# Optimization experiments

Measured on AMD Instinct MI355X. Metric: run time of the kernel, lower is better.

The kernel has to match this reference:

```python
import jax, jax.numpy as jnp
import numpy as np
from itertools import product

N = 300000          # active voxels
CIN, C = 16, 32     # input / conv channels
K = 27              # 3x3x3 kernel volume
Z, Y, X = 41, 1024, 1024  # sparse spatial shape (grid_size[::-1] + [1,0,0])
B = 2               # batch size
EPS = 1e-3          # BatchNorm eps (matches norm_fn eps=0.001)


def _build_coords_and_rulebook(rng):
    # unique active coords per batch element
    total = Z * Y * X
    per = N // B
    coords = []
    for b in range(B):
        lin = np.unique(rng.integers(0, total, size=int(per * 1.3)))
        rng.shuffle(lin)
        lin = lin[:per]
        assert lin.shape[0] == per
        z = lin // (Y * X)
        y = (lin % (Y * X)) // X
        x = lin % X
        coords.append(np.stack([np.full(per, b), z, y, x], axis=1))
    coords = np.concatenate(coords, axis=0).astype(np.int64)  # [N,4]

    # hash-free rulebook via sorted linear keys + searchsorted
    key = ((coords[:, 0] * Z + coords[:, 1]) * Y + coords[:, 2]) * X + coords[:, 3]
    perm = np.argsort(key)
    skey = key[perm]
    nbr = np.full((N, K), -1, dtype=np.int32)
    bz, zz, yy, xx = coords[:, 0], coords[:, 1], coords[:, 2], coords[:, 3]
    for k, (dz, dy, dx) in enumerate(product((-1, 0, 1), repeat=3)):
        nz, ny, nx = zz + dz, yy + dy, xx + dx
        valid = (nz >= 0) & (nz < Z) & (ny >= 0) & (ny < Y) & (nx >= 0) & (nx < X)
        nkey = ((bz * Z + nz) * Y + ny) * X + nx
        pos = np.searchsorted(skey, nkey)
        pos = np.clip(pos, 0, N - 1)
        found = valid & (skey[pos] == nkey)
        nbr[:, k] = np.where(found, perm[pos], -1).astype(np.int32)
    return coords, nbr


def _bn_params(k, c):
    k1, k2, k3, k4 = jax.random.split(k, 4)
    gamma = jax.random.uniform(k1, (c,), minval=0.5, maxval=1.5)
    beta = jax.random.normal(k2, (c,)) * 0.1
    mean = jax.random.normal(k3, (c,)) * 0.1
    var = jax.random.uniform(k4, (c,), minval=0.5, maxval=1.5)
    return jnp.stack([gamma, beta, mean, var], axis=0)  # [4,C]


def setup_inputs() -> dict:
    rng = np.random.default_rng(0)
    _, nbr = _build_coords_and_rulebook(rng)

    key = jax.random.key(0)
    ks = jax.random.split(key, 12)
    feat = jax.random.normal(ks[0], (N, CIN), dtype=jnp.float32)

    def conv_w(k, cin, cout):
        return jax.random.normal(k, (K, cin, cout), dtype=jnp.float32) * (1.0 / np.sqrt(K * cin))

    return {
        "voxel_features": feat,
        "neighbor_idx": jnp.asarray(nbr),
        "w_in": conv_w(ks[1], CIN, C), "bn_in": _bn_params(ks[2], C),
        "w1a": conv_w(ks[3], C, C), "bn1a": _bn_params(ks[4], C),
        "w1b": conv_w(ks[5], C, C), "bn1b": _bn_params(ks[6], C),
        "w2a": conv_w(ks[7], C, C), "bn2a": _bn_params(ks[8], C),
        "w2b": conv_w(ks[9], C, C), "bn2b": _bn_params(ks[10], C),
    }


def reference(voxel_features, neighbor_idx, w_in, bn_in, w1a, bn1a, w1b, bn1b,
              w2a, bn2a, w2b, bn2b):
    def bn(x, p):
        gamma, beta, mean, var = p
        return gamma * (x - mean) * jax.lax.rsqrt(var + EPS) + beta

    def subm(feat, w):
        # submanifold conv: gather active neighbors, GEMM per kernel offset, accumulate
        out = jnp.zeros((feat.shape[0], w.shape[2]), feat.dtype)
        for k in range(K):
            idx = neighbor_idx[:, k]
            g = jnp.where((idx >= 0)[:, None], feat[jnp.maximum(idx, 0)], 0.0)
            out = out + g @ w[k]
        return out

    # conv_input: SubMConv3d + BN + ReLU
    x = jax.nn.relu(bn(subm(voxel_features, w_in), bn_in))
    # conv1: two SparseBasicBlocks (conv-bn-relu-conv-bn + residual, relu)
    for wa, bna, wb, bnb in ((w1a, bn1a, w1b, bn1b), (w2a, bn2a, w2b, bn2b)):
        identity = x
        x = jax.nn.relu(bn(subm(x, wa), bna))
        x = bn(subm(x, wb), bnb)
        x = jax.nn.relu(x + identity)
    # voxel importance (vis_importance branch, minus file IO / sorting side effects)
    voxel_importance = jax.nn.sigmoid(jnp.mean(jnp.abs(x), axis=1, keepdims=True))
    return x, voxel_importance
```

## Files before the change

### kernel.cpp

```cpp
#include <hip/hip_runtime.h>
#include <hip/hip_bf16.h>
#include <hip/hip_fp16.h>
#include <cstdint>
#include <cstddef>

#define NVOX 300000
#define KNBR 27
#define COUT 32
#define CINP 32
#define NT   (NVOX / 16)
#define RB   ((NVOX + 255) / 256)
#define WFIXE (5 * KNBR * CINP * COUT)
#define WFB  ((WFIXE + 255) / 256)
#define WDE  (5 * COUT * CINP)
#define WDB  ((WDE + 255) / 256)
#define WDK  (5 * KNBR * CINP * COUT)
#define WKB  ((WDK + 255) / 256)
#define WPL  (KNBR * CINP * COUT)
#define GD   1792
#define GF0  256
#define GC1  512
#define GP   256
#define PCAP 150016

typedef __hip_bfloat16 bf16;
typedef _Float16 half8 __attribute__((ext_vector_type(8)));
typedef float floatx4 __attribute__((ext_vector_type(4)));
typedef unsigned short ushort8 __attribute__((ext_vector_type(8)));

__device__ __forceinline__ float bf2f(unsigned short u) {
    union { unsigned int i; float f; } x; x.i = ((unsigned int)u) << 16; return x.f;
}
__device__ __forceinline__ int detect_fp32(const void* b0) {
    const unsigned short* p = (const unsigned short*)b0;
    int hits = 0;
    for (int i = 0; i < 16; i++) {
        float v = bf2f(p[2 * i]);
        if (v >= 0.25f && v <= 4.0f) hits++;
    }
    return (hits >= 8) ? 0 : 1;
}
__device__ __forceinline__ float rdw(const void* w, int rel, int fp32) {
    return fp32 ? ((const float*)w)[rel] : __bfloat162float(((const bf16*)w)[rel]);
}


__global__ __launch_bounds__(256)
void setup_kernel(const int* __restrict__ nbr,
                  const void* w0, const void* w1, const void* w2, const void* w3, const void* w4,
                  const void* b0, const void* b1, const void* b2, const void* b3, const void* b4,
                  float* __restrict__ wfix, __half* __restrict__ wtf, __half* __restrict__ wtk,
                  float* __restrict__ bnab,
                  int* __restrict__ flag, int* __restrict__ counter,
                  int* __restrict__ cvlist, int* __restrict__ corrpos,
                  unsigned char* __restrict__ nnarr, int* __restrict__ pk1) {
    const int tid = threadIdx.x;

    if (blockIdx.x < RB) {
        __shared__ int flags[256];
        __shared__ int pk1s[256];
        __shared__ int wsum[4];
        __shared__ int wbase[4];
        flags[tid] = 0;
        __syncthreads();
        const int base = blockIdx.x * 256;
        const int nvox = (NVOX - base < 256) ? (NVOX - base) : 256;
        const int nI4  = (nvox * KNBR) >> 2;
        const int4* p4 = (const int4*)(nbr + (size_t)base * KNBR);
        for (int i = tid; i < nI4; i += 256) {
            const int4 q = p4[i];
            if ((q.x & q.y & q.z & q.w) < 0) continue;
            const unsigned t = (unsigned)(i << 2);
            if (q.x >= 0) { unsigned u = t;     unsigned lv = (u * 4855u) >> 17; unsigned kk = u - lv * 27u; if (kk != 13u) { atomicAdd(&flags[lv], 1); pk1s[lv] = (int)((kk << 19) | (unsigned)q.x); } }
            if (q.y >= 0) { unsigned u = t + 1; unsigned lv = (u * 4855u) >> 17; unsigned kk = u - lv * 27u; if (kk != 13u) { atomicAdd(&flags[lv], 1); pk1s[lv] = (int)((kk << 19) | (unsigned)q.y); } }
            if (q.z >= 0) { unsigned u = t + 2; unsigned lv = (u * 4855u) >> 17; unsigned kk = u - lv * 27u; if (kk != 13u) { atomicAdd(&flags[lv], 1); pk1s[lv] = (int)((kk << 19) | (unsigned)q.z); } }
            if (q.w >= 0) { unsigned u = t + 3; unsigned lv = (u * 4855u) >> 17; unsigned kk = u - lv * 27u; if (kk != 13u) { atomicAdd(&flags[lv], 1); pk1s[lv] = (int)((kk << 19) | (unsigned)q.w); } }
        }
        __syncthreads();
        const int v = base + tid;
        const int nn = flags[tid];
        const bool inr = (tid < nvox);
        if (inr) nnarr[v] = (unsigned char)(nn > 255 ? 255 : nn);
        if (inr && nn == 1) pk1[v] = pk1s[tid];
        const bool f = inr && (nn > 0);
        const unsigned long long wm = __ballot(f);
        const int wd = tid >> 6, ln = tid & 63;
        if (ln == 0) wsum[wd] = __popcll(wm);
        __syncthreads();
        if (tid == 0) {
            int t0 = wsum[0], t1 = wsum[1], t2 = wsum[2], t3 = wsum[3];
            int tot = t0 + t1 + t2 + t3;
            int b = tot ? atomicAdd(counter, tot) : 0;
            wbase[0] = b; wbase[1] = b + t0; wbase[2] = b + t0 + t1; wbase[3] = b + t0 + t1 + t2;
        }
        __syncthreads();
        if (f) {
            int pos = wbase[wd] + __popcll(wm & ((1ULL << ln) - 1ULL));
            cvlist[pos] = v;
            corrpos[v]  = pos;
        }
        return;
    }

    const int fp32 = detect_fp32(b0);

    if (blockIdx.x < RB + WFB) {
        int i = (blockIdx.x - RB) * 256 + tid;
        if (i >= WFIXE) return;
        int L   = i / (KNBR * CINP * COUT);
        int rem = i % (KNBR * CINP * COUT);
        int k   = rem / (CINP * COUT);
        int kk  = (rem / COUT) % CINP;
        int nn  = rem % COUT;
        const void* w = (L == 0) ? w0 : (L == 1) ? w1 : (L == 2) ? w2 : (L == 3) ? w3 : w4;
        int cinL = (L == 0) ? 16 : 32;
        wfix[i] = (kk < cinL) ? rdw(w, (k * cinL + kk) * COUT + nn, fp32) : 0.f;
        return;
    }

    if (blockIdx.x < RB + WFB + WDB) {
        int i = (blockIdx.x - RB - WFB) * 256 + tid;
        if (i >= WDE) return;
        int L  = i / (COUT * CINP);
        int nn = (i / CINP) % COUT;
        int kk = i % CINP;
        const void* w = (L == 0) ? w0 : (L == 1) ? w1 : (L == 2) ? w2 : (L == 3) ? w3 : w4;
        int cinL = (L == 0) ? 16 : 32;
        int sk = (L == 0) ? kk : ((kk & 1) ? 16 + (kk >> 1) : (kk >> 1));
        float val = (sk < cinL) ? rdw(w, (13 * cinL + sk) * COUT + nn, fp32) : 0.f;
        wtf[i] = __float2half(val);
        return;
    }

    if (blockIdx.x < RB + WFB + WDB + WKB) {
        int i = (blockIdx.x - RB - WFB - WDB) * 256 + tid;
        if (i >= WDK) return;
        int L   = i / (KNBR * CINP * COUT);
        int rem = i % (KNBR * CINP * COUT);
        int k   = rem / (CINP * COUT);
        int nn  = (rem / CINP) % COUT;
        int kk  = rem % CINP;
        const void* w = (L == 0) ? w0 : (L == 1) ? w1 : (L == 2) ? w2 : (L == 3) ? w3 : w4;
        int cinL = (L == 0) ? 16 : 32;
        int sk = (L == 0) ? kk : ((kk & 1) ? 16 + (kk >> 1) : (kk >> 1));
        float val = (sk < cinL) ? rdw(w, (k * cinL + sk) * COUT + nn, fp32) : 0.f;
        wtk[i] = __float2half(val);
        return;
    }

    if (tid == 192) *flag = fp32;
    if (tid < 160) {
        int L = tid / 32, c = tid % 32;
        const void* b = (L == 0) ? b0 : (L == 1) ? b1 : (L == 2) ? b2 : (L == 3) ? b3 : b4;
        float g, be, m, v;
        if (fp32) {
            const float* q = (const float*)b;
            g = q[c]; be = q[32 + c]; m = q[64 + c]; v = q[96 + c];
        } else {
            const bf16* q = (const bf16*)b;
            g = __bfloat162float(q[c]); be = __bfloat162float(q[32 + c]);
            m = __bfloat162float(q[64 + c]); v = __bfloat162float(q[96 + c]);
        }
        float a = g * rsqrtf(v + 1e-3f);
        bnab[L * 64 + c]      = a;
        bnab[L * 64 + 32 + c] = be - a * m;
    }
}


struct DW {
    half8 wa[5], wb[5];
    float ba[5], bb[5], bc[5], bd[5];
};
__device__ __forceinline__ void load_dw(DW& d, const __half* __restrict__ wtf,
                                        const float* __restrict__ bnab, int n, int quad) {
#pragma unroll
    for (int L = 0; L < 5; L++) {
        d.wa[L] = *(const half8*)((const _Float16*)wtf + L * 1024 + n * 32 + quad * 8);
        d.wb[L] = *(const half8*)((const _Float16*)wtf + L * 1024 + (n + 16) * 32 + quad * 8);
        d.ba[L] = bnab[L * 64 + n];      d.bb[L] = bnab[L * 64 + 32 + n];
        d.bc[L] = bnab[L * 64 + 16 + n]; d.bd[L] = bnab[L * 64 + 48 + n];
    }
}

__device__ __forceinline__ void dense_range(
    int gw, int nw, const DW& dw,
    const void* __restrict__ feat, int fp32, void* __restrict__ out_base,
    _Float16 (* __restrict__ myT)[40], int n, int quad) {
    for (int t = gw; t < NT; t += nw) {
        const int v0 = t * 16;
        half8 af = {};
        if (quad < 2) {
            if (fp32) {
                const float* p = (const float*)feat + (size_t)(v0 + n) * 16 + quad * 8;
                const float4 u0 = *(const float4*)p;
                const float4 u1 = *(const float4*)(p + 4);
                af[0] = (_Float16)u0.x; af[1] = (_Float16)u0.y; af[2] = (_Float16)u0.z; af[3] = (_Float16)u0.w;
                af[4] = (_Float16)u1.x; af[5] = (_Float16)u1.y; af[6] = (_Float16)u1.z; af[7] = (_Float16)u1.w;
            } else {
                const ushort8 u = *(const ushort8*)((const unsigned short*)feat + (size_t)(v0 + n) * 16 + quad * 8);
#pragma unroll
                for (int j = 0; j < 8; j++) af[j] = (_Float16)bf2f(u[j]);
            }
        }
        float id0[4], id1[4];
#pragma unroll
        for (int L = 0; L < 5; L++) {
            floatx4 c0 = {0.f, 0.f, 0.f, 0.f}, c1 = {0.f, 0.f, 0.f, 0.f};
            c0 = __builtin_amdgcn_mfma_f32_16x16x32_f16(af, dw.wa[L], c0, 0, 0, 0);
            c1 = __builtin_amdgcn_mfma_f32_16x16x32_f16(af, dw.wb[L], c1, 0, 0, 0);
            if (L < 4) {
#pragma unroll
                for (int r = 0; r < 4; r++) {
                    float y0 = fmaf(dw.ba[L], c0[r], dw.bb[L]);
                    float y1 = fmaf(dw.bc[L], c1[r], dw.bd[L]);
                    if (L == 2) { y0 += id0[r]; y1 += id1[r]; }
                    y0 = fmaxf(y0, 0.f); y1 = fmaxf(y1, 0.f);
                    if (L == 0 || L == 2) { id0[r] = y0; id1[r] = y1; }
                    const int m = quad * 4 + r;
                    *reinterpret_cast<__half2*>(&myT[m][2 * n]) = __floats2half2_rn(y0, y1);
                }
                af = *reinterpret_cast<const half8*>(&myT[n][quad * 8]);
            } else {
#pragma unroll
                for (int r = 0; r < 4; r++) {
                    float y0 = fmaxf(fmaf(dw.ba[4], c0[r], dw.bb[4]) + id0[r], 0.f);
                    float y1 = fmaxf(fmaf(dw.bc[4], c1[r], dw.bd[4]) + id1[r], 0.f);
                    const int v = v0 + quad * 4 + r;
                    float s = y0 + y1;
#pragma unroll
                    for (int o = 1; o < 16; o <<= 1) s += __shfl_xor(s, o, 16);
                    const float imp = 1.0f / (1.0f + expf(-s * (1.0f / 32.0f)));
                    if (fp32) {
                        float* ox = (float*)out_base;
                        ox[(size_t)v * COUT + n]      = y0;
                        ox[(size_t)v * COUT + n + 16] = y1;
                        if (n == 0) ox[(size_t)NVOX * COUT + v] = imp;
                    } else {
                        bf16* ox = (bf16*)out_base;
                        ox[(size_t)v * COUT + n]      = __float2bfloat16(y0);
                        ox[(size_t)v * COUT + n + 16] = __float2bfloat16(y1);
                        if (n == 0) ox[(size_t)NVOX * COUT + v] = __float2bfloat16(imp);
                    }
                }
            }
        }
    }
}

__device__ __forceinline__ void fix0_range(
    int nC, int wbase0, int wstride, int lane,
    const void* __restrict__ feat, const int* __restrict__ nbr,
    const int* __restrict__ cvlist, const int* __restrict__ corrpos,
    const unsigned char* __restrict__ nnarr, const int* __restrict__ pk1,
    int* __restrict__ ctap, int* __restrict__ clist, int* __restrict__ ccount,
    int* __restrict__ pbuck, int* __restrict__ pcnt13,
    const float* __restrict__ wt, const float* __restrict__ bnab,
    __half* __restrict__ xout, int fp32) {
    const int c = lane & 31;
    const float bna = bnab[c], bnb = bnab[32 + c];
    for (int i0 = wbase0; i0 < nC; i0 += wstride) {
        const int i = i0 + lane;
        const bool inr = i < nC;
        int v = 0; bool pair = false; int u = 0, k = 0;
        if (inr) {
            v = cvlist[i];
            if (nnarr[v] == 1) {
                const int e = pk1[v];
                u = e & 0x7FFFF; k = e >> 19;
                pair = (nnarr[u] == 1);
            }
        }
        const bool emitP = pair && (k < 13);
#pragma unroll
        for (int bb = 0; bb < 13; bb++) {
            const unsigned long long mb = __ballot(emitP && (k == bb));
            if (mb == 0) continue;
            int basep = 0;
            if (lane == 0) basep = atomicAdd(&pcnt13[bb * 16], __popcll(mb));
            basep = __shfl(basep, 0, 64);
            if (emitP && (k == bb)) {
                const int pos = basep + __popcll(mb & ((1ULL << lane) - 1ULL));
                int* pb = pbuck + (size_t)bb * (2 * PCAP);
                pb[2 * pos]     = (v << 5) | k;
                pb[2 * pos + 1] = u;
            }
        }
        const bool cplx = inr && !pair;
        unsigned long long mc = __ballot(cplx);
        const int cc = __popcll(mc);
        int baseC = 0;
        if (lane == 0 && cc) baseC = atomicAdd(ccount, cc);
        baseC = __shfl(baseC, 0, 64);
        if (cplx) clist[baseC + __popcll(mc & ((1ULL << lane) - 1ULL))] = i;

        while (mc) {
            const int l = (int)__builtin_ctzll(mc); mc &= mc - 1;
            const int ii = i0 + l;
            const int vv = __shfl(v, l, 64);
            int idx = (lane < KNBR) ? nbr[(size_t)vv * KNBR + lane] : -1;
            const bool valid = idx >= 0;
            unsigned long long m = __ballot(valid) & ((1ULL << KNBR) - 1ULL);
            if (valid) {
                int sp  = corrpos[idx];
                int pos = __popcll(m & ((1ULL << lane) - 1ULL));
                ctap[(size_t)ii * 28 + 1 + pos] = (sp << 5) | lane;
            }
            if (lane == 0) ctap[(size_t)ii * 28] = __popcll(m);
            float acc0 = 0.f, acc1 = 0.f;
            while (m) {
                const int k0 = (int)__builtin_ctzll(m); m &= m - 1;
                int k1 = -1;
                if (m) { k1 = (int)__builtin_ctzll(m); m &= m - 1; }
                const int kme = (lane >= 32) ? k1 : k0;
                const bool act = (kme >= 0);
                const int kk = act ? kme : 0;
                const int src = __shfl(idx, kk, 64);
                float xv = 0.f;
                if (act && c < 16)
                    xv = fp32 ? ((const float*)feat)[(size_t)src * 16 + c]
                              : bf2f(((const unsigned short*)feat)[(size_t)src * 16 + c]);
                const float* wk = wt + (size_t)kk * (CINP * COUT) + c;
#pragma unroll
                for (int j = 0; j < 16; j += 2) {
                    float xa = __shfl(xv, j, 32);
                    float xb = __shfl(xv, j + 1, 32);
                    acc0 = fmaf(xa, wk[j * COUT], acc0);
                    acc1 = fmaf(xb, wk[(j + 1) * COUT], acc1);
                }
            }
            float acc = acc0 + acc1;
            acc += __shfl_xor(acc, 32, 64);
            float y = fmaxf(fmaf(bna, acc, bnb), 0.f);
            if (lane < 32) xout[(size_t)ii * COUT + c] = __float2half(y);
        }
    }
}

template<int HAS_RES>
__device__ __forceinline__ void fixs_range(
    int gw, int nw, int lane,
    const __half* __restrict__ xin, const int* __restrict__ ctap,
    const int* __restrict__ clist, const int* __restrict__ ccount,
    const float* __restrict__ wt, const float* __restrict__ bnab,
    const __half* __restrict__ res, __half* __restrict__ xout) {
    const int c = lane & 31;
    const int nC = *ccount;
    const float bna = bnab[c], bnb = bnab[32 + c];
    for (int jj = gw; jj < nC; jj += nw) {
        const int i = clist[jj];
        const size_t tb = (size_t)i * 28;
        const int cnt = ctap[tb];
        const int tp  = ctap[tb + 1 + lane];
        float acc0 = 0.f, acc1 = 0.f;
        for (int t = 0; t < cnt; t += 2) {
            const bool actB = (t + 1) < cnt;
            const int sel = (lane >= 32 && actB) ? (t + 1) : t;
            const int tap = __shfl(tp, sel, 64);
            const bool act = (lane < 32) || actB;
            const int sp = tap >> 5, kk = tap & 31;
            const float xv = act ? __half2float(xin[(size_t)sp * COUT + c]) : 0.f;
            const float* wk = wt + (size_t)kk * (CINP * COUT) + c;
#pragma unroll
            for (int j = 0; j < 32; j += 2) {
                acc0 = fmaf(__shfl(xv, j, 32),     wk[j * COUT],       acc0);
                acc1 = fmaf(__shfl(xv, j + 1, 32), wk[(j + 1) * COUT], acc1);
            }
        }
        float acc = acc0 + acc1;
        acc += __shfl_xor(acc, 32, 64);
        float y = fmaf(bna, acc, bnb);
        if (HAS_RES) y += __half2float(res[(size_t)i * COUT + c]);
        y = fmaxf(y, 0.f);
        if (lane < 32) xout[(size_t)i * COUT + c] = __float2half(y);
    }
}

__device__ __forceinline__ void pairs_range(
    int gw, int nw, int lane,
    const void* __restrict__ feat,
    const int* __restrict__ pcnt13, const int* __restrict__ pbuck,
    const __half* __restrict__ wtk, const float* __restrict__ bnab,
    void* __restrict__ out_base, int fp32,
    _Float16 (* __restrict__ Tv)[40], _Float16 (* __restrict__ Tu)[40]) {
    const int n = lane & 15, quad = lane >> 4;
    int G = 0;
#pragma unroll
    for (int bb = 0; bb < 13; bb++) G += (pcnt13[bb * 16] + 15) >> 4;

    for (int gi = gw; gi < G; gi += nw) {
        int b = 0, g = 0, nb = 0;
        {
            int acc = 0, found = 0;
#pragma unroll
            for (int bb = 0; bb < 13; bb++) {
                const int cbb = pcnt13[bb * 16];
                const int ng = (cbb + 15) >> 4;
                if (!found && gi < acc + ng) { b = bb; g = gi - acc; nb = cbb; found = 1; }
                acc += ng;
            }
        }
        const int* pb = pbuck + (size_t)b * (2 * PCAP);
        const int base = g * 16;
        int rA = base + n; if (rA > nb - 1) rA = nb - 1;
        const int vA = pb[2 * rA] >> 5;
        const int uA = pb[2 * rA + 1];

        half8 afv = {}, afu = {};
        if (quad < 2) {
            if (fp32) {
                const float* pv = (const float*)feat + (size_t)vA * 16 + quad * 8;
                const float* pu = (const float*)feat + (size_t)uA * 16 + quad * 8;
                const float4 v0 = *(const float4*)pv, v1 = *(const float4*)(pv + 4);
                const float4 u0 = *(const float4*)pu, u1 = *(const float4*)(pu + 4);
                afv[0] = (_Float16)v0.x; afv[1] = (_Float16)v0.y; afv[2] = (_Float16)v0.z; afv[3] = (_Float16)v0.w;
                afv[4] = (_Float16)v1.x; afv[5] = (_Float16)v1.y; afv[6] = (_Float16)v1.z; afv[7] = (_Float16)v1.w;
                afu[0] = (_Float16)u0.x; afu[1] = (_Float16)u0.y; afu[2] = (_Float16)u0.z; afu[3] = (_Float16)u0.w;
                afu[4] = (_Float16)u1.x; afu[5] = (_Float16)u1.y; afu[6] = (_Float16)u1.z; afu[7] = (_Float16)u1.w;
            } else {
                const ushort8 sv = *(const ushort8*)((const unsigned short*)feat + (size_t)vA * 16 + quad * 8);
                const ushort8 su = *(const ushort8*)((const unsigned short*)feat + (size_t)uA * 16 + quad * 8);
#pragma unroll
                for (int j = 0; j < 8; j++) { afv[j] = (_Float16)bf2f(sv[j]); afu[j] = (_Float16)bf2f(su[j]); }
            }
        }
        float idv0[4], idv1[4], idu0[4], idu1[4];
#pragma unroll
        for (int L = 0; L < 5; L++) {
            const _Float16* w13 = (const _Float16*)wtk + (size_t)(L * 27 + 13) * 1024;
            const _Float16* wkb = (const _Float16*)wtk + (size_t)(L * 27 + b) * 1024;
            const _Float16* wqb = (const _Float16*)wtk + (size_t)(L * 27 + (26 - b)) * 1024;
            const half8 B13a = *(const half8*)(w13 + n * 32 + quad * 8);
            const half8 B13b = *(const half8*)(w13 + (n + 16) * 32 + quad * 8);
            const half8 Bka  = *(const half8*)(wkb + n * 32 + quad * 8);
            const half8 Bkb  = *(const half8*)(wkb + (n + 16) * 32 + quad * 8);
            const half8 Bqa  = *(const half8*)(wqb + n * 32 + quad * 8);
            const half8 Bqb  = *(const half8*)(wqb + (n + 16) * 32 + quad * 8);
            const float a0 = bnab[L * 64 + n],      c0b = bnab[L * 64 + 32 + n];
            const float a1 = bnab[L * 64 + 16 + n], c1b = bnab[L * 64 + 48 + n];
            floatx4 cv0 = {0.f,0.f,0.f,0.f}, cv1 = {0.f,0.f,0.f,0.f};
            floatx4 cu0 = {0.f,0.f,0.f,0.f}, cu1 = {0.f,0.f,0.f,0.f};
            cv0 = __builtin_amdgcn_mfma_f32_16x16x32_f16(afv, B13a, cv0, 0, 0, 0);
            cv0 = __builtin_amdgcn_mfma_f32_16x16x32_f16(afu, Bka,  cv0, 0, 0, 0);
            cv1 = __builtin_amdgcn_mfma_f32_16x16x32_f16(afv, B13b, cv1, 0, 0, 0);
            cv1 = __builtin_amdgcn_mfma_f32_16x16x32_f16(afu, Bkb,  cv1, 0, 0, 0);
            cu0 = __builtin_amdgcn_mfma_f32_16x16x32_f16(afu, B13a, cu0, 0, 0, 0);
            cu0 = __builtin_amdgcn_mfma_f32_16x16x32_f16(afv, Bqa,  cu0, 0, 0, 0);
            cu1 = __builtin_amdgcn_mfma_f32_16x16x32_f16(afu, B13b, cu1, 0, 0, 0);
            cu1 = __builtin_amdgcn_mfma_f32_16x16x32_f16(afv, Bqb,  cu1, 0, 0, 0);
            if (L < 4) {
#pragma unroll
                for (int r = 0; r < 4; r++) {
                    float yv0 = fmaf(a0, cv0[r], c0b), yv1 = fmaf(a1, cv1[r], c1b);
                    float yu0 = fmaf(a0, cu0[r], c0b), yu1 = fmaf(a1, cu1[r], c1b);
                    if (L == 2) { yv0 += idv0[r]; yv1 += idv1[r]; yu0 += idu0[r]; yu1 += idu1[r]; }
                    yv0 = fmaxf(yv0, 0.f); yv1 = fmaxf(yv1, 0.f);
                    yu0 = fmaxf(yu0, 0.f); yu1 = fmaxf(yu1, 0.f);
                    if (L == 0 || L == 2) { idv0[r] = yv0; idv1[r] = yv1; idu0[r] = yu0; idu1[r] = yu1; }
                    const int m = quad * 4 + r;
                    *reinterpret_cast<__half2*>(&Tv[m][2 * n]) = __floats2half2_rn(yv0, yv1);
                    *reinterpret_cast<__half2*>(&Tu[m][2 * n]) = __floats2half2_rn(yu0, yu1);
                }
                afv = *reinterpret_cast<const half8*>(&Tv[n][quad * 8]);
                afu = *reinterpret_cast<const half8*>(&Tu[n][quad * 8]);
            } else {
#pragma unroll
                for (int r = 0; r < 4; r++) {
                    const int m = quad * 4 + r;
                    const int im = base + m;
                    const bool valid = im < nb;
                    const int ri = valid ? im : (nb - 1);
                    const int vm = pb[2 * ri] >> 5;
                    const int um = pb[2 * ri + 1];
                    float yv0 = fmaxf(fmaf(a0, cv0[r], c0b) + idv0[r], 0.f);
                    float yv1 = fmaxf(fmaf(a1, cv1[r], c1b) + idv1[r], 0.f);
                    float yu0 = fmaxf(fmaf(a0, cu0[r], c0b) + idu0[r], 0.f);
                    float yu1 = fmaxf(fmaf(a1, cu1[r], c1b) + idu1[r], 0.f);
                    float sv = yv0 + yv1, su = yu0 + yu1;
#pragma unroll
                    for (int o = 1; o < 16; o <<= 1) { sv += __shfl_xor(sv, o, 16); su += __shfl_xor(su, o, 16); }
                    const float impv = 1.0f / (1.0f + expf(-sv * (1.0f / 32.0f)));
                    const float impu = 1.0f / (1.0f + expf(-su * (1.0f / 32.0f)));
                    if (valid) {
                        if (fp32) {
                            float* ox = (float*)out_base;
                            ox[(size_t)vm * COUT + n]      = yv0;
                            ox[(size_t)vm * COUT + n + 16] = yv1;
                            ox[(size_t)um * COUT + n]      = yu0;
                            ox[(size_t)um * COUT + n + 16] = yu1;
                            if (n == 0) { ox[(size_t)NVOX * COUT + vm] = impv; ox[(size_t)NVOX * COUT + um] = impu; }
                        } else {
                            bf16* ox = (bf16*)out_base;
                            ox[(size_t)vm * COUT + n]      = __float2bfloat16(yv0);
                            ox[(size_t)vm * COUT + n + 16] = __float2bfloat16(yv1);
                            ox[(size_t)um * COUT + n]      = __float2bfloat16(yu0);
                            ox[(size_t)um * COUT + n + 16] = __float2bfloat16(yu1);
                            if (n == 0) { ox[(size_t)NVOX * COUT + vm] = __float2bfloat16(impv); ox[(size_t)NVOX * COUT + um] = __float2bfloat16(impu); }
                        }
                    }
                }
            }
        }
    }
}


__global__ __launch_bounds__(256)
void phase0_kernel(const void* __restrict__ feat, const int* __restrict__ nbr,
                   const int* __restrict__ cvlist, const int* __restrict__ corrpos,
                   const unsigned char* __restrict__ nnarr, const int* __restrict__ pk1,
                   const int* __restrict__ counter, int* __restrict__ ctap,
                   int* __restrict__ clist, int* __restrict__ ccount,
                   int* __restrict__ pbuck, int* __restrict__ pcnt13,
                   const float* __restrict__ wfix, const __half* __restrict__ wtf,
                   const float* __restrict__ bnab,
                   __half* __restrict__ Xc0, void* __restrict__ out_base,
                   const int* __restrict__ flag) {
    __shared__ __align__(16) _Float16 ldsT[4][16][40];
    const int lane = threadIdx.x & 63;
    const int fp32 = *flag;
    if (blockIdx.x < GD) {
        const int gw = (blockIdx.x * 256 + threadIdx.x) >> 6;
        const int nw = (GD * 256) >> 6;
        const int wv = threadIdx.x >> 6;
        const int n = lane & 15, quad = lane >> 4;
        DW dw; load_dw(dw, wtf, bnab, n, quad);
        dense_range(gw, nw, dw, feat, fp32, out_base, ldsT[wv], n, quad);
    } else {
        const int wb = (blockIdx.x - GD) * 256 + (threadIdx.x & ~63);
        fix0_range(*counter, wb, GF0 * 256, lane, feat, nbr, cvlist, corrpos,
                   nnarr, pk1, ctap, clist, ccount, pbuck, pcnt13,
                   wfix, bnab, Xc0, fp32);
    }
}

__global__ __launch_bounds__(256)
void stage1_kernel(const void* __restrict__ feat,
                   const __half* __restrict__ Xc0, const int* __restrict__ ctap,
                   const int* __restrict__ clist, const int* __restrict__ ccount,
                   const int* __restrict__ pcnt13, const int* __restrict__ pbuck,
                   const __half* __restrict__ wtk,
                   const float* __restrict__ wfixL1, const float* __restrict__ bnabL1,
                   const float* __restrict__ bnab,
                   __half* __restrict__ Xc1, void* __restrict__ out_base,
                   const int* __restrict__ flag) {
    __shared__ __align__(16) _Float16 T[4][2][16][40];
    const int lane = threadIdx.x & 63;
    if (blockIdx.x < GC1) {
        const int gw = (blockIdx.x * 256 + threadIdx.x) >> 6;
        const int nw = (GC1 * 256) >> 6;
        fixs_range<0>(gw, nw, lane, Xc0, ctap, clist, ccount, wfixL1, bnabL1, nullptr, Xc1);
    } else {
        const int gw = ((blockIdx.x - GC1) * 256 + threadIdx.x) >> 6;
        const int nw = (GP * 256) >> 6;
        const int wv = threadIdx.x >> 6;
        pairs_range(gw, nw, lane, feat, pcnt13, pbuck, wtk, bnab,
                    out_base, *flag, T[wv][0], T[wv][1]);
    }
}

template<int HAS_RES>
__global__ __launch_bounds__(256)
void fixs_kernel(const __half* __restrict__ xin, const int* __restrict__ ctap,
                 const int* __restrict__ clist, const int* __restrict__ ccount,
                 const float* __restrict__ wt, const float* __restrict__ bnab,
                 const __half* __restrict__ res, __half* __restrict__ xout) {
    const int gw   = (blockIdx.x * 256 + threadIdx.x) >> 6;
    const int nw   = (gridDim.x * 256) >> 6;
    const int lane = threadIdx.x & 63;
    fixs_range<HAS_RES>(gw, nw, lane, xin, ctap, clist, ccount, wt, bnab, res, xout);
}

__global__ __launch_bounds__(256)
void final_kernel(const int* __restrict__ clist, const int* __restrict__ ccount,
                  const int* __restrict__ ctap, const int* __restrict__ cvlist,
                  const __half* __restrict__ Xc1, const __half* __restrict__ Xc2,
                  const float* __restrict__ wfix, const float* __restrict__ bnab,
                  void* __restrict__ out_base, const int* __restrict__ flag) {
    const int gw   = (blockIdx.x * 256 + threadIdx.x) >> 6;
    const int nw   = (gridDim.x * 256) >> 6;
    const int lane = threadIdx.x & 63;
    const int c    = lane & 31;
    const int ncplx = *ccount;
    const int fp32io = *flag;

    for (int j = gw; j < ncplx; j += nw) {
        const int i = clist[j];
        const size_t tb = (size_t)i * 28;
        const int cnt = ctap[tb];
        const int tp  = ctap[tb + 1 + lane];
        const float* wt = wfix + 4 * WPL;
        float acc0 = 0.f, acc1 = 0.f;
        for (int t = 0; t < cnt; t += 2) {
            const bool actB = (t + 1) < cnt;
            const int sel = (lane >= 32 && actB) ? (t + 1) : t;
            const int tap = __shfl(tp, sel, 64);
            const bool act = (lane < 32) || actB;
            const int sp = tap >> 5, kk = tap & 31;
            const float xv = act ? __half2float(Xc1[(size_t)sp * COUT + c]) : 0.f;
            const float* wk = wt + (size_t)kk * (CINP * COUT) + c;
#pragma unroll
            for (int jq = 0; jq < 32; jq += 2) {
                acc0 = fmaf(__shfl(xv, jq, 32),     wk[jq * COUT],       acc0);
                acc1 = fmaf(__shfl(xv, jq + 1, 32), wk[(jq + 1) * COUT], acc1);
            }
        }
        float acc = acc0 + acc1;
        acc += __shfl_xor(acc, 32, 64);
        float y = fmaf(bnab[4 * 64 + c], acc, bnab[4 * 64 + 32 + c]);
        y += __half2float(Xc2[(size_t)i * COUT + c]);
        y = fmaxf(y, 0.f);
        float s2 = y;
#pragma unroll
        for (int o = 16; o > 0; o >>= 1) s2 += __shfl_xor(s2, o, 32);
        const float imp = 1.0f / (1.0f + expf(-s2 * (1.0f / 32.0f)));
        const int v = cvlist[i];
        if (fp32io) {
            float* ox = (float*)out_base;
            if (lane < 32) ox[(size_t)v * COUT + c] = y;
            if (lane == 0) ox[(size_t)NVOX * COUT + v] = imp;
        } else {
            bf16* ox = (bf16*)out_base;
            if (lane < 32) ox[(size_t)v * COUT + c] = __float2bfloat16(y);
            if (lane == 0) ox[(size_t)NVOX * COUT + v] = __float2bfloat16(imp);
        }
    }
}

extern "C" void kernel_launch(void* const* d_in, const int* in_sizes, int n_in,
                              void* d_out, int out_size, void* d_ws, size_t ws_size,
                              hipStream_t stream) {
    char* ws = (char*)d_ws;
    int*    counter = (int*)ws;
    int*    flag    = counter + 1;
    int*    ccount  = counter + 3;
    int*    pcnt13  = (int*)(ws + 256);
    int*    cvlist  = (int*)(ws + 1280);
    int*    corrpos = cvlist + NVOX;
    int*    clist   = corrpos + NVOX;
    int*    pk1     = clist + NVOX;
    unsigned char* nnarr = (unsigned char*)(pk1 + NVOX);
    uintptr_t pa    = (((uintptr_t)(nnarr + NVOX)) + 255) & ~(uintptr_t)255;
    int*    ctap    = (int*)pa;
    int*    pbuck   = ctap + (size_t)NVOX * 28 + 64;
    float*  wfix    = (float*)(pbuck + (size_t)13 * PCAP * 2);
    float*  bnab    = wfix + WFIXE;
    __half* wtf     = (__half*)(bnab + 320);
    __half* wtk     = wtf + WDE;
    uintptr_t xa    = (((uintptr_t)(wtk + WDK)) + 255) & ~(uintptr_t)255;
    __half* Xc0 = (__half*)xa;
    __half* Xc1 = Xc0 + (size_t)NVOX * COUT;
    __half* Xc2 = Xc1 + (size_t)NVOX * COUT;

    const void* feat = d_in[0];
    const int*  nbr  = (const int*)d_in[1];

    hipMemsetAsync(ws, 0, 1088, stream);

    setup_kernel<<<dim3(RB + WFB + WDB + WKB + 1), 256, 0, stream>>>(
        nbr, d_in[2], d_in[4], d_in[6], d_in[8], d_in[10],
        d_in[3], d_in[5], d_in[7], d_in[9], d_in[11],
        wfix, wtf, wtk, bnab, flag, counter, cvlist, corrpos, nnarr, pk1);

    phase0_kernel<<<dim3(GD + GF0), 256, 0, stream>>>(
        feat, nbr, cvlist, corrpos, nnarr, pk1, counter, ctap, clist, ccount,
        pbuck, pcnt13, wfix, wtf, bnab, Xc0, d_out, flag);

    stage1_kernel<<<dim3(GC1 + GP), 256, 0, stream>>>(
        feat, Xc0, ctap, clist, ccount, pcnt13, pbuck, wtk,
        wfix + 1 * WPL, bnab + 1 * 64, bnab, Xc1, d_out, flag);

    dim3 gs(512);
    fixs_kernel<1><<<gs, 256, 0, stream>>>(Xc1, ctap, clist, ccount, wfix + 2 * WPL, bnab + 2 * 64, Xc0, Xc2);
    fixs_kernel<0><<<gs, 256, 0, stream>>>(Xc2, ctap, clist, ccount, wfix + 3 * WPL, bnab + 3 * 64, nullptr, Xc1);

    final_kernel<<<dim3(512), 256, 0, stream>>>(
        clist, ccount, ctap, cvlist, Xc1, Xc2, wfix, bnab, d_out, flag);
}
```

Before: 197.9 us.

## Split complex-voxel layer-0 conv out of classification into stage1 wave-per-voxel pass

```diff
diff --git a/kernel.cpp b/kernel.cpp
--- a/kernel.cpp
+++ b/kernel.cpp
@@ -17,9 +17,9 @@
 #define WDK  (5 * KNBR * CINP * COUT)
 #define WKB  ((WDK + 255) / 256)
 #define WPL  (KNBR * CINP * COUT)
-#define GD   1792
-#define GF0  256
-#define GC1  512
+#define GD   1984
+#define GF0  64
+#define GC0  512
 #define GP   256
 #define PCAP 150016
 
@@ -248,17 +248,12 @@
     }
 }
 
-__device__ __forceinline__ void fix0_range(
+__device__ __forceinline__ void classify_range(
     int nC, int wbase0, int wstride, int lane,
-    const void* __restrict__ feat, const int* __restrict__ nbr,
-    const int* __restrict__ cvlist, const int* __restrict__ corrpos,
+    const int* __restrict__ cvlist,
     const unsigned char* __restrict__ nnarr, const int* __restrict__ pk1,
-    int* __restrict__ ctap, int* __restrict__ clist, int* __restrict__ ccount,
-    int* __restrict__ pbuck, int* __restrict__ pcnt13,
-    const float* __restrict__ wt, const float* __restrict__ bnab,
-    __half* __restrict__ xout, int fp32) {
-    const int c = lane & 31;
-    const float bna = bnab[c], bnb = bnab[32 + c];
+    int* __restrict__ clist, int* __restrict__ ccount,
+    int* __restrict__ pbuck, int* __restrict__ pcnt13) {
     for (int i0 = wbase0; i0 < nC; i0 += wstride) {
         const int i = i0 + lane;
         const bool inr = i < nC;
@@ -287,53 +282,64 @@
             }
         }
         const bool cplx = inr && !pair;
-        unsigned long long mc = __ballot(cplx);
+        const unsigned long long mc = __ballot(cplx);
         const int cc = __popcll(mc);
         int baseC = 0;
         if (lane == 0 && cc) baseC = atomicAdd(ccount, cc);
         baseC = __shfl(baseC, 0, 64);
         if (cplx) clist[baseC + __popcll(mc & ((1ULL << lane) - 1ULL))] = i;
-
-        while (mc) {
-            const int l = (int)__builtin_ctzll(mc); mc &= mc - 1;
-            const int ii = i0 + l;
-            const int vv = __shfl(v, l, 64);
-            int idx = (lane < KNBR) ? nbr[(size_t)vv * KNBR + lane] : -1;
-            const bool valid = idx >= 0;
-            unsigned long long m = __ballot(valid) & ((1ULL << KNBR) - 1ULL);
-            if (valid) {
-                int sp  = corrpos[idx];
-                int pos = __popcll(m & ((1ULL << lane) - 1ULL));
-                ctap[(size_t)ii * 28 + 1 + pos] = (sp << 5) | lane;
-            }
-            if (lane == 0) ctap[(size_t)ii * 28] = __popcll(m);
-            float acc0 = 0.f, acc1 = 0.f;
-            while (m) {
-                const int k0 = (int)__builtin_ctzll(m); m &= m - 1;
-                int k1 = -1;
-                if (m) { k1 = (int)__builtin_ctzll(m); m &= m - 1; }
-                const int kme = (lane >= 32) ? k1 : k0;
-                const bool act = (kme >= 0);
-                const int kk = act ? kme : 0;
-                const int src = __shfl(idx, kk, 64);
-                float xv = 0.f;
-                if (act && c < 16)
-                    xv = fp32 ? ((const float*)feat)[(size_t)src * 16 + c]
-                              : bf2f(((const unsigned short*)feat)[(size_t)src * 16 + c]);
-                const float* wk = wt + (size_t)kk * (CINP * COUT) + c;
-#pragma unroll
-                for (int j = 0; j < 16; j += 2) {
-                    float xa = __shfl(xv, j, 32);
-                    float xb = __shfl(xv, j + 1, 32);
-                    acc0 = fmaf(xa, wk[j * COUT], acc0);
-                    acc1 = fmaf(xb, wk[(j + 1) * COUT], acc1);
-                }
-            }
-            float acc = acc0 + acc1;
-            acc += __shfl_xor(acc, 32, 64);
-            float y = fmaxf(fmaf(bna, acc, bnb), 0.f);
-            if (lane < 32) xout[(size_t)ii * COUT + c] = __float2half(y);
-        }
+    }
+}
+
+__device__ __forceinline__ void cplx0_range(
+    int gw, int nw, int lane,
+    const void* __restrict__ feat, const int* __restrict__ nbr,
+    const int* __restrict__ cvlist, const int* __restrict__ corrpos,
+    const int* __restrict__ clist, const int* __restrict__ ccount,
+    int* __restrict__ ctap,
+    const float* __restrict__ wt, const float* __restrict__ bnab,
+    __half* __restrict__ xout, int fp32) {
+    const int c = lane & 31;
+    const int nC = *ccount;
+    const float bna = bnab[c], bnb = bnab[32 + c];
+    for (int jj = gw; jj < nC; jj += nw) {
+        const int ii = clist[jj];
+        const int vv = cvlist[ii];
+        int idx = (lane < KNBR) ? nbr[(size_t)vv * KNBR + lane] : -1;
+        const bool valid = idx >= 0;
+        unsigned long long m = __ballot(valid) & ((1ULL << KNBR) - 1ULL);
+        if (valid) {
+            int sp  = corrpos[idx];
+            int pos = __popcll(m & ((1ULL << lane) - 1ULL));
+            ctap[(size_t)ii * 28 + 1 + pos] = (sp << 5) | lane;
+        }
+        if (lane == 0) ctap[(size_t)ii * 28] = __popcll(m);
+        float acc0 = 0.f, acc1 = 0.f;
+        while (m) {
+            const int k0 = (int)__builtin_ctzll(m); m &= m - 1;
+            int k1 = -1;
+            if (m) { k1 = (int)__builtin_ctzll(m); m &= m - 1; }
+            const int kme = (lane >= 32) ? k1 : k0;
+            const bool act = (kme >= 0);
+            const int kk = act ? kme : 0;
+            const int src = __shfl(idx, kk, 64);
+            float xv = 0.f;
+            if (act && c < 16)
+                xv = fp32 ? ((const float*)feat)[(size_t)src * 16 + c]
+                          : bf2f(((const unsigned short*)feat)[(size_t)src * 16 + c]);
+            const float* wk = wt + (size_t)kk * (CINP * COUT) + c;
+#pragma unroll
+            for (int j = 0; j < 16; j += 2) {
+                float xa = __shfl(xv, j, 32);
+                float xb = __shfl(xv, j + 1, 32);
+                acc0 = fmaf(xa, wk[j * COUT], acc0);
+                acc1 = fmaf(xb, wk[(j + 1) * COUT], acc1);
+            }
+        }
+        float acc = acc0 + acc1;
+        acc += __shfl_xor(acc, 32, 64);
+        float y = fmaxf(fmaf(bna, acc, bnb), 0.f);
+        if (lane < 32) xout[(size_t)ii * COUT + c] = __float2half(y);
     }
 }
 
@@ -506,16 +512,14 @@
 
 
 __global__ __launch_bounds__(256)
-void phase0_kernel(const void* __restrict__ feat, const int* __restrict__ nbr,
-                   const int* __restrict__ cvlist, const int* __restrict__ corrpos,
+void phase0_kernel(const void* __restrict__ feat,
+                   const int* __restrict__ cvlist,
                    const unsigned char* __restrict__ nnarr, const int* __restrict__ pk1,
-                   const int* __restrict__ counter, int* __restrict__ ctap,
+                   const int* __restrict__ counter,
                    int* __restrict__ clist, int* __restrict__ ccount,
                    int* __restrict__ pbuck, int* __restrict__ pcnt13,
-                   const float* __restrict__ wfix, const __half* __restrict__ wtf,
-                   const float* __restrict__ bnab,
-                   __half* __restrict__ Xc0, void* __restrict__ out_base,
-                   const int* __restrict__ flag) {
+                   const __half* __restrict__ wtf, const float* __restrict__ bnab,
+                   void* __restrict__ out_base, const int* __restrict__ flag) {
     __shared__ __align__(16) _Float16 ldsT[4][16][40];
     const int lane = threadIdx.x & 63;
     const int fp32 = *flag;
@@ -528,34 +532,36 @@
         dense_range(gw, nw, dw, feat, fp32, out_base, ldsT[wv], n, quad);
     } else {
         const int wb = (blockIdx.x - GD) * 256 + (threadIdx.x & ~63);
-        fix0_range(*counter, wb, GF0 * 256, lane, feat, nbr, cvlist, corrpos,
-                   nnarr, pk1, ctap, clist, ccount, pbuck, pcnt13,
-                   wfix, bnab, Xc0, fp32);
+        classify_range(*counter, wb, GF0 * 256, lane, cvlist, nnarr, pk1,
+                       clist, ccount, pbuck, pcnt13);
     }
 }
 
 __global__ __launch_bounds__(256)
-void stage1_kernel(const void* __restrict__ feat,
-                   const __half* __restrict__ Xc0, const int* __restrict__ ctap,
+void stage1_kernel(const void* __restrict__ feat, const int* __restrict__ nbr,
+                   const int* __restrict__ cvlist, const int* __restrict__ corrpos,
                    const int* __restrict__ clist, const int* __restrict__ ccount,
+                   int* __restrict__ ctap,
                    const int* __restrict__ pcnt13, const int* __restrict__ pbuck,
                    const __half* __restrict__ wtk,
-                   const float* __restrict__ wfixL1, const float* __restrict__ bnabL1,
+                   const float* __restrict__ wfixL0, const float* __restrict__ bnabL0,
                    const float* __restrict__ bnab,
-                   __half* __restrict__ Xc1, void* __restrict__ out_base,
+                   __half* __restrict__ Xc0, void* __restrict__ out_base,
                    const int* __restrict__ flag) {
     __shared__ __align__(16) _Float16 T[4][2][16][40];
     const int lane = threadIdx.x & 63;
-    if (blockIdx.x < GC1) {
+    const int fp32 = *flag;
+    if (blockIdx.x < GC0) {
         const int gw = (blockIdx.x * 256 + threadIdx.x) >> 6;
-        const int nw = (GC1 * 256) >> 6;
-        fixs_range<0>(gw, nw, lane, Xc0, ctap, clist, ccount, wfixL1, bnabL1, nullptr, Xc1);
+        const int nw = (GC0 * 256) >> 6;
+        cplx0_range(gw, nw, lane, feat, nbr, cvlist, corrpos, clist, ccount,
+                    ctap, wfixL0, bnabL0, Xc0, fp32);
     } else {
-        const int gw = ((blockIdx.x - GC1) * 256 + threadIdx.x) >> 6;
+        const int gw = ((blockIdx.x - GC0) * 256 + threadIdx.x) >> 6;
         const int nw = (GP * 256) >> 6;
         const int wv = threadIdx.x >> 6;
         pairs_range(gw, nw, lane, feat, pcnt13, pbuck, wtk, bnab,
-                    out_base, *flag, T[wv][0], T[wv][1]);
+                    out_base, fp32, T[wv][0], T[wv][1]);
     }
 }
 
@@ -663,14 +669,15 @@
         wfix, wtf, wtk, bnab, flag, counter, cvlist, corrpos, nnarr, pk1);
 
     phase0_kernel<<<dim3(GD + GF0), 256, 0, stream>>>(
-        feat, nbr, cvlist, corrpos, nnarr, pk1, counter, ctap, clist, ccount,
-        pbuck, pcnt13, wfix, wtf, bnab, Xc0, d_out, flag);
-
-    stage1_kernel<<<dim3(GC1 + GP), 256, 0, stream>>>(
-        feat, Xc0, ctap, clist, ccount, pcnt13, pbuck, wtk,
-        wfix + 1 * WPL, bnab + 1 * 64, bnab, Xc1, d_out, flag);
+        feat, cvlist, nnarr, pk1, counter, clist, ccount, pbuck, pcnt13,
+        wtf, bnab, d_out, flag);
+
+    stage1_kernel<<<dim3(GC0 + GP), 256, 0, stream>>>(
+        feat, nbr, cvlist, corrpos, clist, ccount, ctap, pcnt13, pbuck, wtk,
+        wfix + 0 * WPL, bnab + 0 * 64, bnab, Xc0, d_out, flag);
 
     dim3 gs(512);
+    fixs_kernel<0><<<gs, 256, 0, stream>>>(Xc0, ctap, clist, ccount, wfix + 1 * WPL, bnab + 1 * 64, nullptr, Xc1);
     fixs_kernel<1><<<gs, 256, 0, stream>>>(Xc1, ctap, clist, ccount, wfix + 2 * WPL, bnab + 2 * 64, Xc0, Xc2);
     fixs_kernel<0><<<gs, 256, 0, stream>>>(Xc2, ctap, clist, ccount, wfix + 3 * WPL, bnab + 3 * 64, nullptr, Xc1);
 
```

After: 191.5 us. 1.03x faster.
